# Kernel tuning notes

Hardware: AMD Instinct MI355X
Metric: run time of the kernel (lower is better)

The kernel has to match this reference:

```python
import jax, jax.numpy as jnp
import numpy as np

B, N, H = 512, 128, 256      # graphs, nodes per graph, hidden
NH, HD = 8, 32               # heads, head dim
DEG = 8
E = B * N * DEG              # 524288 edges
BN_EPS = 1e-5


def setup_inputs() -> dict:
    key = jax.random.key(0)
    ks = jax.random.split(key, 16)

    def w(k, shape):
        return jax.random.normal(k, shape, dtype=jnp.float32) * 0.02

    # intra-graph random edges: base offset per graph, local src/dst in [0, N)
    base = jnp.repeat(jnp.arange(B, dtype=jnp.int32) * N, N * DEG)
    edge_src = base + jax.random.randint(ks[1], (E,), 0, N, dtype=jnp.int32)
    edge_dst = base + jax.random.randint(ks[2], (E,), 0, N, dtype=jnp.int32)

    return {
        "h": jax.random.normal(ks[0], (B * N, H), dtype=jnp.float32),
        "edge_src": edge_src,
        "edge_dst": edge_dst,
        "gin_w1": w(ks[3], (H, H)), "gin_b1": jnp.zeros((H,), jnp.float32),
        "gin_w2": w(ks[4], (H, H)), "gin_b2": jnp.zeros((H,), jnp.float32),
        "attn_in_w": w(ks[5], (3 * H, H)), "attn_in_b": jnp.zeros((3 * H,), jnp.float32),
        "attn_out_w": w(ks[6], (H, H)), "attn_out_b": jnp.zeros((H,), jnp.float32),
        "bn_local_g": jnp.ones((H,), jnp.float32), "bn_local_b": jnp.zeros((H,), jnp.float32),
        "bn_attn_g": jnp.ones((H,), jnp.float32), "bn_attn_b": jnp.zeros((H,), jnp.float32),
        "bn_out_g": jnp.ones((H,), jnp.float32), "bn_out_b": jnp.zeros((H,), jnp.float32),
        "ffn1_w": w(ks[7], (2 * H, H)), "ffn1_b": jnp.zeros((2 * H,), jnp.float32),
        "ffn2_w": w(ks[8], (H, 2 * H)), "ffn2_b": jnp.zeros((H,), jnp.float32),
    }


def _bn(x, g, b):
    # nn.BatchNorm1d training-mode forward: batch stats over node dim, biased var
    mean = jnp.mean(x, axis=0)
    var = jnp.mean(jnp.square(x - mean), axis=0)
    return g * (x - mean) * jax.lax.rsqrt(var + BN_EPS) + b


def _mha(x, in_w, in_b, out_w, out_b):
    # x: [B, N, H]; uniform graphs -> key_padding_mask is all-valid
    qkv = x @ in_w.T + in_b                           # [B, N, 3H]
    q, k, v = jnp.split(qkv, 3, axis=-1)
    def heads(t):
        return t.reshape(B, N, NH, HD).transpose(0, 2, 1, 3)  # [B, NH, N, HD]
    q, k, v = heads(q), heads(k), heads(v)
    scores = jnp.einsum('bhqd,bhkd->bhqk', q, k) / jnp.sqrt(jnp.float32(HD))
    att = jax.nn.softmax(scores, axis=-1)
    o = jnp.einsum('bhqk,bhkd->bhqd', att, v).transpose(0, 2, 1, 3).reshape(B, N, H)
    return o @ out_w.T + out_b


def reference(h, edge_src, edge_dst,
              gin_w1, gin_b1, gin_w2, gin_b2,
              attn_in_w, attn_in_b, attn_out_w, attn_out_b,
              bn_local_g, bn_local_b, bn_attn_g, bn_attn_b, bn_out_g, bn_out_b,
              ffn1_w, ffn1_b, ffn2_w, ffn2_b):
    # --- local GIN branch: (1+eps)*h + sum_{j in N(i)} h_j, eps=0, then 2-layer MLP
    agg = jax.ops.segment_sum(h[edge_src], edge_dst, num_segments=B * N)
    z = h + agg
    h_local = jax.nn.relu(z @ gin_w1.T + gin_b1) @ gin_w2.T + gin_b2
    h_local = _bn(h + h_local, bn_local_g, bn_local_b)

    # --- global attention branch (to_dense_batch is an exact reshape here)
    h_dense = h.reshape(B, N, H)
    h_attn = _mha(h_dense, attn_in_w, attn_in_b, attn_out_w, attn_out_b).reshape(B * N, H)
    h_attn = _bn(h + h_attn, bn_attn_g, bn_attn_b)

    # --- combine + FFN + out norm
    x = h_local + h_attn
    x = x + jax.nn.relu(x @ ffn1_w.T + ffn1_b) @ ffn2_w.T + ffn2_b
    return _bn(x, bn_out_g, bn_out_b)
```

## Files before the change

kernel.cpp:

```cpp
#include <hip/hip_runtime.h>
#include <hip/hip_bf16.h>

#define B_   512
#define N_   128
#define H_   256
#define NH_  8
#define HD_  32
#define DEG_ 8
#define R_   (B_ * N_)
#define E_   (B_ * N_ * DEG_)
#define EPG_ (N_ * DEG_)

typedef unsigned short u16;
typedef unsigned int u32;

typedef __attribute__((ext_vector_type(8))) short s16x8;
typedef __attribute__((ext_vector_type(4))) float f32x4;

__device__ __forceinline__ float b2f(u16 u) {
  union { u32 i; float f; } v;
  v.i = ((u32)u) << 16;
  return v.f;
}
__device__ __forceinline__ u16 f2b(float f) {
  union { float f; u32 u; } v;
  v.f = f;
  u32 r = (v.u + 0x7fffu + ((v.u >> 16) & 1u)) >> 16;
  return (u16)r;
}
__device__ __forceinline__ void ld4b(const u16* p, float* o) {
  ushort4 v = *(const ushort4*)p;
  o[0] = b2f(v.x); o[1] = b2f(v.y); o[2] = b2f(v.z); o[3] = b2f(v.w);
}


#define OFF_GW1 0
#define OFF_GB1 65536
#define OFF_GW2 65792
#define OFF_GB2 131328
#define OFF_AIW 131584
#define OFF_AIB 328192
#define OFF_AOW 328960
#define OFF_AOB 394496
#define OFF_F1W 394752
#define OFF_F1B 525824
#define OFF_F2W 526336
#define OFF_F2B 657408
#define W_TOTAL 657664

__global__ void zero_stats(float* __restrict__ st) {
  st[blockIdx.x * 256 + threadIdx.x] = 0.f;
}

__global__ __launch_bounds__(256) void cvt_h(const float* __restrict__ src,
                                             u16* __restrict__ dst) {
  const size_t i = ((size_t)blockIdx.x * 256 + threadIdx.x) * 4;
  const float4 v = *(const float4*)(src + i);
  ushort4 o;
  o.x = f2b(v.x); o.y = f2b(v.y); o.z = f2b(v.z); o.w = f2b(v.w);
  *(ushort4*)(dst + i) = o;
}

__global__ __launch_bounds__(256) void cvt_w(
    const float* s0, const float* s1, const float* s2, const float* s3,
    const float* s4, const float* s5, const float* s6, const float* s7,
    const float* s8, const float* s9, const float* s10, const float* s11,
    u16* __restrict__ dst) {
  const int sizes[12] = {65536, 256, 65536, 256, 196608, 768,
                         65536, 256, 131072, 512, 131072, 256};
  const float* srcs[12] = {s0, s1, s2, s3, s4, s5, s6, s7, s8, s9, s10, s11};
  int gid = (blockIdx.x * 256 + threadIdx.x) * 4;
  if (gid >= W_TOTAL) return;
  int seg = 0, off = gid;
  while (off >= sizes[seg]) { off -= sizes[seg]; seg++; }
  const float4 v = *(const float4*)(srcs[seg] + off);
  ushort4 o;
  o.x = f2b(v.x); o.y = f2b(v.y); o.z = f2b(v.z); o.w = f2b(v.w);
  *(ushort4*)(dst + gid) = o;
}

#define SROWS_ 32

__global__ __launch_bounds__(256) void agg_kernel(
    const u16* __restrict__ h, const int* __restrict__ esrc,
    const int* __restrict__ edst, u16* __restrict__ z) {
  __shared__ int s_src[EPG_];
  __shared__ int s_cnt[SROWS_];
  __shared__ int s_off[SROWS_ + 1];
  __shared__ int s_pos[SROWS_];
  const int g = blockIdx.x;
  const int r0 = blockIdx.y * SROWS_;
  const int t = threadIdx.x;

  if (t < SROWS_) s_cnt[t] = 0;
  __syncthreads();

  const int ebase = g * EPG_;
  int dl[4], sg[4];
#pragma unroll
  for (int i = 0; i < 4; i++) {
    const int e = ebase + t + i * 256;
    sg[i] = esrc[e];
    dl[i] = edst[e] - g * N_ - r0;
    if ((unsigned)dl[i] < SROWS_) atomicAdd(&s_cnt[dl[i]], 1);
  }
  __syncthreads();
  if (t == 0) {
    int acc = 0;
#pragma unroll
    for (int i = 0; i < SROWS_; i++) { s_off[i] = acc; acc += s_cnt[i]; }
    s_off[SROWS_] = acc;
  }
  __syncthreads();
  if (t < SROWS_) s_pos[t] = s_off[t];
  __syncthreads();
#pragma unroll
  for (int i = 0; i < 4; i++) {
    if ((unsigned)dl[i] < SROWS_) {
      const int slot = atomicAdd(&s_pos[dl[i]], 1);
      s_src[slot] = sg[i];
    }
  }
  __syncthreads();

  const int rg = t >> 5;
  const int c0 = (t & 31) * 8;
  for (int ib = 0; ib < SROWS_; ib += 8) {
    const int i = ib + rg;
    const int row = g * N_ + r0 + i;
    float acc[8];
    {
      const s16x8 v = *(const s16x8*)(h + (size_t)row * H_ + c0);
#pragma unroll
      for (int j = 0; j < 8; j++) acc[j] = b2f((u16)v[j]);
    }
    const int e0 = s_off[i], e1 = s_off[i + 1];
    for (int e = e0; e < e1; e++) {
      const int src = s_src[e];
      const s16x8 v = *(const s16x8*)(h + (size_t)src * H_ + c0);
#pragma unroll
      for (int j = 0; j < 8; j++) acc[j] += b2f((u16)v[j]);
    }
    s16x8 o;
#pragma unroll
    for (int j = 0; j < 8; j++) o[j] = (short)f2b(acc[j]);
    *(s16x8*)(z + (size_t)row * H_ + c0) = o;
  }
}

template <int NC, int K, int RELU, int RES, int STATS, int ASPLIT, int CMODE>
__global__ __launch_bounds__(256) void gemm_mfma(
    const u16* A, const u16* A2,
    const u16* __restrict__ W, const u16* __restrict__ bias,
    const u16* res, u16* C0, u16* C1, u16* C2,
    float* __restrict__ gsum, float* __restrict__ gsq) {
  __shared__ u16 As[2][128 * 64] __attribute__((aligned(16)));
  __shared__ u16 Bs[2][128 * 64] __attribute__((aligned(16)));

  const int t = threadIdx.x;
  const int wave = t >> 6, lane = t & 63;
  const int wr = wave >> 1, wc = wave & 1;
  const int quad = lane >> 4, ln15 = lane & 15;
  const int row0 = blockIdx.x * 128, col0 = blockIdx.y * 128;

  f32x4 acc[4][4];
#pragma unroll
  for (int i = 0; i < 4; i++)
#pragma unroll
    for (int j = 0; j < 4; j++) acc[i][j] = (f32x4){0.f, 0.f, 0.f, 0.f};

  auto stage = [&](int b, int kt) {
#pragma unroll
    for (int i = 0; i < 4; i++) {
      const int fid = t + i * 256;
      const int row = fid >> 3;
      const int segp = (fid & 7) ^ (row & 7);
      const u16* Ab;
      int kb;
      if (ASPLIT) {
        if (kt < 256) { Ab = A; kb = kt; } else { Ab = A2; kb = kt - 256; }
      } else {
        Ab = A; kb = kt;
      }
      const int astr = ASPLIT ? 256 : K;
      const u16* ga = Ab + (size_t)(row0 + row) * astr + kb + segp * 8;
      __builtin_amdgcn_global_load_lds(
          (const __attribute__((address_space(1))) void*)ga,
          (__attribute__((address_space(3))) void*)(&As[b][fid * 8]), 16, 0, 0);
      const u16* gw = W + (size_t)(col0 + row) * K + kt + segp * 8;
      __builtin_amdgcn_global_load_lds(
          (const __attribute__((address_space(1))) void*)gw,
          (__attribute__((address_space(3))) void*)(&Bs[b][fid * 8]), 16, 0, 0);
    }
  };

  stage(0, 0);
  for (int kt = 0; kt < K; kt += 64) {
    const int cur = (kt >> 6) & 1;
    if (kt + 64 < K) {
      stage(cur ^ 1, kt + 64);
      asm volatile("s_waitcnt vmcnt(8)" ::: "memory");
    } else {
      asm volatile("s_waitcnt vmcnt(0)" ::: "memory");
    }
    __builtin_amdgcn_s_barrier();
#pragma unroll
    for (int ks = 0; ks < 64; ks += 32) {
      s16x8 af[4], bf[4];
#pragma unroll
      for (int i = 0; i < 4; i++) {
        const int ra = wr * 64 + i * 16 + ln15;
        af[i] = *(const s16x8*)(
            &As[cur][ra * 64 + ((((ks >> 3) + quad) ^ (ra & 7)) * 8)]);
      }
#pragma unroll
      for (int j = 0; j < 4; j++) {
        const int rb = wc * 64 + j * 16 + ln15;
        bf[j] = *(const s16x8*)(
            &Bs[cur][rb * 64 + ((((ks >> 3) + quad) ^ (rb & 7)) * 8)]);
      }
#pragma unroll
      for (int i = 0; i < 4; i++)
#pragma unroll
        for (int j = 0; j < 4; j++)
          acc[i][j] = __builtin_amdgcn_mfma_f32_16x16x32_bf16(af[i], bf[j], acc[i][j], 0, 0, 0);
    }
    __builtin_amdgcn_s_barrier();
  }

  const int cbase = col0 + wc * 64;
  u16* Cb;
  int coff, cstr;
  if (CMODE) {
    const int chunk = col0 >> 8;
    Cb = (chunk == 0) ? C0 : ((chunk == 1) ? C1 : C2);
    coff = (col0 & 255) + wc * 64;
    cstr = 256;
  } else {
    Cb = C0; coff = cbase; cstr = NC;
  }

  float bs[4];
#pragma unroll
  for (int j = 0; j < 4; j++) bs[j] = b2f(bias[cbase + j * 16 + ln15]);

  float ssum[4] = {}, ssq[4] = {};
#pragma unroll
  for (int i = 0; i < 4; i++) {
    const int rbase = row0 + wr * 64 + i * 16 + quad * 4;
#pragma unroll
    for (int reg = 0; reg < 4; reg++) {
      const int row = rbase + reg;
#pragma unroll
      for (int j = 0; j < 4; j++) {
        float val = acc[i][j][reg] + bs[j];
        if (RELU) val = fmaxf(val, 0.f);
        if (RES) val += b2f(res[(size_t)row * 256 + cbase + j * 16 + ln15]);
        Cb[(size_t)row * cstr + coff + j * 16 + ln15] = f2b(val);
        if (STATS) { ssum[j] += val; ssq[j] += val * val; }
      }
    }
  }

  if (STATS) {
#pragma unroll
    for (int j = 0; j < 4; j++) {
      float s = ssum[j];
      s += __shfl_xor(s, 16);
      s += __shfl_xor(s, 32);
      float q = ssq[j];
      q += __shfl_xor(q, 16);
      q += __shfl_xor(q, 32);
      if (lane < 16) {
        atomicAdd(&gsum[cbase + j * 16 + lane], s);
        atomicAdd(&gsq[cbase + j * 16 + lane], q);
      }
    }
  }
}

__global__ __launch_bounds__(256) void attn_mfma(
    const u16* q, const u16* __restrict__ k,
    const u16* __restrict__ v, u16* o) {
  __shared__ u16 lds[21760] __attribute__((aligned(16)));
  u16* Vt = lds;
  u16* Qs = lds + 4352;
  u16* Ks = lds + 4352 + 5120;
  u16* P  = lds + 4352;

  const int g = blockIdx.x >> 3;
  const int hd = blockIdx.x & 7;
  const int t = threadIdx.x;
  const int wave = t >> 6, lane = t & 63;
  const int quad = lane >> 4, ln15 = lane & 15;
  const int strip = wave * 32;
  const float scale = 0.1767766952966369f;

#pragma unroll
  for (int i = 0; i < 4; i++) {
    const int fid = t + i * 256;
    const int row = fid >> 3;
    const int seg = fid & 7;
    const size_t gidx = (size_t)(g * N_ + row) * H_ + hd * HD_ + seg * 4;
    const ushort4 qv = *(const ushort4*)(q + gidx);
    const ushort4 kv = *(const ushort4*)(k + gidx);
    const ushort4 vv = *(const ushort4*)(v + gidx);
    ushort4 qs;
    qs.x = f2b(b2f(qv.x) * scale); qs.y = f2b(b2f(qv.y) * scale);
    qs.z = f2b(b2f(qv.z) * scale); qs.w = f2b(b2f(qv.w) * scale);
    *(ushort4*)(Qs + row * 40 + seg * 4) = qs;
    *(ushort4*)(Ks + row * 40 + seg * 4) = kv;
    Vt[(seg * 4 + 0) * 136 + row] = vv.x;
    Vt[(seg * 4 + 1) * 136 + row] = vv.y;
    Vt[(seg * 4 + 2) * 136 + row] = vv.z;
    Vt[(seg * 4 + 3) * 136 + row] = vv.w;
  }
  __syncthreads();

  s16x8 af[2], bf[8];
#pragma unroll
  for (int mi = 0; mi < 2; mi++)
    af[mi] = *(const s16x8*)(Qs + (strip + mi * 16 + ln15) * 40 + quad * 8);
#pragma unroll
  for (int nj = 0; nj < 8; nj++)
    bf[nj] = *(const s16x8*)(Ks + (nj * 16 + ln15) * 40 + quad * 8);

  f32x4 acc[2][8];
#pragma unroll
  for (int mi = 0; mi < 2; mi++)
#pragma unroll
    for (int nj = 0; nj < 8; nj++)
      acc[mi][nj] = __builtin_amdgcn_mfma_f32_16x16x32_bf16(
          af[mi], bf[nj], (f32x4){0.f, 0.f, 0.f, 0.f}, 0, 0, 0);

  __syncthreads();

#pragma unroll
  for (int mi = 0; mi < 2; mi++) {
#pragma unroll
    for (int reg = 0; reg < 4; reg++) {
      float mx = acc[mi][0][reg];
#pragma unroll
      for (int j = 1; j < 8; j++) mx = fmaxf(mx, acc[mi][j][reg]);
      mx = fmaxf(mx, __shfl_xor(mx, 1));
      mx = fmaxf(mx, __shfl_xor(mx, 2));
      mx = fmaxf(mx, __shfl_xor(mx, 4));
      mx = fmaxf(mx, __shfl_xor(mx, 8));
      float e[8], s = 0.f;
#pragma unroll
      for (int j = 0; j < 8; j++) { e[j] = __expf(acc[mi][j][reg] - mx); s += e[j]; }
      s += __shfl_xor(s, 1);
      s += __shfl_xor(s, 2);
      s += __shfl_xor(s, 4);
      s += __shfl_xor(s, 8);
      const float inv = 1.f / s;
      const int prow = strip + mi * 16 + quad * 4 + reg;
#pragma unroll
      for (int j = 0; j < 8; j++)
        P[prow * 136 + j * 16 + ln15] = f2b(e[j] * inv);
    }
  }
  __syncthreads();

  f32x4 acc2[2][2];
#pragma unroll
  for (int mi = 0; mi < 2; mi++)
#pragma unroll
    for (int nj = 0; nj < 2; nj++) acc2[mi][nj] = (f32x4){0.f, 0.f, 0.f, 0.f};
#pragma unroll
  for (int kt = 0; kt < 4; kt++) {
    s16x8 paf[2], vbf[2];
#pragma unroll
    for (int mi = 0; mi < 2; mi++)
      paf[mi] = *(const s16x8*)(P + (strip + mi * 16 + ln15) * 136 + kt * 32 + quad * 8);
#pragma unroll
    for (int nj = 0; nj < 2; nj++)
      vbf[nj] = *(const s16x8*)(Vt + (nj * 16 + ln15) * 136 + kt * 32 + quad * 8);
#pragma unroll
    for (int mi = 0; mi < 2; mi++)
#pragma unroll
      for (int nj = 0; nj < 2; nj++)
        acc2[mi][nj] = __builtin_amdgcn_mfma_f32_16x16x32_bf16(
            paf[mi], vbf[nj], acc2[mi][nj], 0, 0, 0);
  }

#pragma unroll
  for (int mi = 0; mi < 2; mi++)
#pragma unroll
    for (int nj = 0; nj < 2; nj++)
#pragma unroll
      for (int reg = 0; reg < 4; reg++) {
        const int row = strip + mi * 16 + quad * 4 + reg;
        o[(size_t)(g * N_ + row) * H_ + hd * HD_ + nj * 16 + ln15] =
            f2b(acc2[mi][nj][reg]);
      }
}

__global__ void bn_finalize(const float* __restrict__ sum,
                            const float* __restrict__ sq,
                            const float* __restrict__ g,
                            const float* __restrict__ bb,
                            float* __restrict__ a, float* __restrict__ b) {
  const int c = threadIdx.x;
  const float mean = sum[c] * (1.f / R_);
  const float var = fmaxf(sq[c] * (1.f / R_) - mean * mean, 0.f);
  const float ai = g[c] * rsqrtf(var + 1e-5f);
  a[c] = ai;
  b[c] = bb[c] - mean * ai;
}

__global__ __launch_bounds__(256) void combine_kernel(
    const u16* __restrict__ rl, const u16* __restrict__ ra,
    const float* __restrict__ st, u16* __restrict__ x) {
  const size_t i = (size_t)blockIdx.x * 256 + threadIdx.x;
  const int col = (int)(i & 63) * 4;
  float rl4[4], ra4[4];
  ld4b(rl + i * 4, rl4);
  ld4b(ra + i * 4, ra4);
  const float* al = st + 1536;
  const float* bl = st + 1792;
  const float* aa = st + 2048;
  const float* ba = st + 2304;
  ushort4 o;
  u16* ov = (u16*)&o;
#pragma unroll
  for (int j = 0; j < 4; j++)
    ov[j] = f2b(al[col + j] * rl4[j] + bl[col + j] + aa[col + j] * ra4[j] + ba[col + j]);
  *(ushort4*)(x + i * 4) = o;
}

__global__ __launch_bounds__(256) void final_kernel(
    const u16* __restrict__ y, const float* __restrict__ st,
    float* __restrict__ out) {
  const size_t i = (size_t)blockIdx.x * 256 + threadIdx.x;
  const int col = (int)(i & 63) * 4;
  float y4[4];
  ld4b(y + i * 4, y4);
  const float* ao = st + 2560;
  const float* bo = st + 2816;
  float4 o;
  o.x = ao[col + 0] * y4[0] + bo[col + 0];
  o.y = ao[col + 1] * y4[1] + bo[col + 1];
  o.z = ao[col + 2] * y4[2] + bo[col + 2];
  o.w = ao[col + 3] * y4[3] + bo[col + 3];
  *(float4*)(out + i * 4) = o;
}

extern "C" void kernel_launch(void* const* d_in, const int* in_sizes, int n_in,
                              void* d_out, int out_size, void* d_ws, size_t ws_size,
                              hipStream_t stream) {
  const float* h = (const float*)d_in[0];
  const int* esrc = (const int*)d_in[1];
  const int* edst = (const int*)d_in[2];
  const float* bn_local_g = (const float*)d_in[11];
  const float* bn_local_b = (const float*)d_in[12];
  const float* bn_attn_g = (const float*)d_in[13];
  const float* bn_attn_b = (const float*)d_in[14];
  const float* bn_out_g = (const float*)d_in[15];
  const float* bn_out_b = (const float*)d_in[16];

  const size_t RH = (size_t)R_ * H_;
  float* stats = (float*)d_ws;
  u16* WB = (u16*)((char*)d_ws + 65536);
  u16* Hb = (u16*)((char*)d_ws + 65536 + 2097152);
  u16* S1 = Hb + RH;
  u16* S2 = S1 + RH;
  u16* OD = (u16*)d_out;
  float* outf = (float*)d_out;

  zero_stats<<<12, 256, 0, stream>>>(stats);
  cvt_h<<<(int)(RH / 4 / 256), 256, 0, stream>>>(h, Hb);
  cvt_w<<<(W_TOTAL / 4 + 255) / 256, 256, 0, stream>>>(
      (const float*)d_in[3], (const float*)d_in[4], (const float*)d_in[5],
      (const float*)d_in[6], (const float*)d_in[7], (const float*)d_in[8],
      (const float*)d_in[9], (const float*)d_in[10], (const float*)d_in[17],
      (const float*)d_in[18], (const float*)d_in[19], (const float*)d_in[20], WB);

  gemm_mfma<768, 256, 0, 0, 0, 0, 1><<<dim3(512, 6), 256, 0, stream>>>(
      Hb, nullptr, WB + OFF_AIW, WB + OFF_AIB, nullptr, S1, S2, OD, nullptr, nullptr);
  attn_mfma<<<B_ * NH_, 256, 0, stream>>>(S1, S2, OD, S1);
  gemm_mfma<256, 256, 0, 1, 1, 0, 0><<<dim3(512, 2), 256, 0, stream>>>(
      S1, nullptr, WB + OFF_AOW, WB + OFF_AOB, Hb, S2, nullptr, nullptr,
      stats + 512, stats + 768);
  agg_kernel<<<dim3(B_, 4), 256, 0, stream>>>(Hb, esrc, edst, OD);
  gemm_mfma<256, 256, 1, 0, 0, 0, 0><<<dim3(512, 2), 256, 0, stream>>>(
      OD, nullptr, WB + OFF_GW1, WB + OFF_GB1, nullptr, S1, nullptr, nullptr,
      nullptr, nullptr);
  gemm_mfma<256, 256, 0, 1, 1, 0, 0><<<dim3(512, 2), 256, 0, stream>>>(
      S1, nullptr, WB + OFF_GW2, WB + OFF_GB2, Hb, OD, nullptr, nullptr,
      stats + 0, stats + 256);

  bn_finalize<<<1, 256, 0, stream>>>(stats + 0, stats + 256, bn_local_g,
                                     bn_local_b, stats + 1536, stats + 1792);
  bn_finalize<<<1, 256, 0, stream>>>(stats + 512, stats + 768, bn_attn_g,
                                     bn_attn_b, stats + 2048, stats + 2304);

  combine_kernel<<<(int)(RH / 4 / 256), 256, 0, stream>>>(OD, S2, stats, S1);
  gemm_mfma<512, 256, 1, 0, 0, 0, 1><<<dim3(512, 4), 256, 0, stream>>>(
      S1, nullptr, WB + OFF_F1W, WB + OFF_F1B, nullptr, S2, OD, nullptr,
      nullptr, nullptr);
  gemm_mfma<256, 512, 0, 1, 1, 1, 0><<<dim3(512, 2), 256, 0, stream>>>(
      S2, OD, WB + OFF_F2W, WB + OFF_F2B, S1, S1, nullptr, nullptr,
      stats + 1024, stats + 1280);

  bn_finalize<<<1, 256, 0, stream>>>(stats + 1024, stats + 1280, bn_out_g,
                                     bn_out_b, stats + 2560, stats + 2816);
  final_kernel<<<(int)(RH / 4 / 256), 256, 0, stream>>>(S1, stats, outf);
}
```

Baseline: 608.6 us.

## Store bf16 activations in GEMM-tile swizzled layout for contiguous A staging

Result: no change. 612.9 us (+0.7%).

```diff
diff --git a/kernel.cpp b/kernel.cpp
--- a/kernel.cpp
+++ b/kernel.cpp
@@ -31,6 +31,11 @@
 __device__ __forceinline__ void ld4b(const u16* p, float* o) {
   ushort4 v = *(const ushort4*)p;
   o[0] = b2f(v.x); o[1] = b2f(v.y); o[2] = b2f(v.z); o[3] = b2f(v.w);
+}
+
+__device__ __forceinline__ int tix(int row, int col) {
+  return ((row >> 7) << 15) + (((col >> 6) & 3) << 13) + ((row & 127) << 6) +
+         (((((col >> 3) & 7) ^ (row & 7))) << 3) + (col & 7);
 }
 
 
@@ -54,11 +59,11 @@
 
 __global__ __launch_bounds__(256) void cvt_h(const float* __restrict__ src,
                                              u16* __restrict__ dst) {
-  const size_t i = ((size_t)blockIdx.x * 256 + threadIdx.x) * 4;
-  const float4 v = *(const float4*)(src + i);
+  const int e = (blockIdx.x * 256 + threadIdx.x) * 4;
+  const float4 v = *(const float4*)(src + e);
   ushort4 o;
   o.x = f2b(v.x); o.y = f2b(v.y); o.z = f2b(v.z); o.w = f2b(v.w);
-  *(ushort4*)(dst + i) = o;
+  *(ushort4*)(dst + tix(e >> 8, e & 255)) = o;
 }
 
 __global__ __launch_bounds__(256) void cvt_w(
@@ -130,21 +135,21 @@
     const int row = g * N_ + r0 + i;
     float acc[8];
     {
-      const s16x8 v = *(const s16x8*)(h + (size_t)row * H_ + c0);
+      const s16x8 v = *(const s16x8*)(h + tix(row, c0));
 #pragma unroll
       for (int j = 0; j < 8; j++) acc[j] = b2f((u16)v[j]);
     }
     const int e0 = s_off[i], e1 = s_off[i + 1];
     for (int e = e0; e < e1; e++) {
       const int src = s_src[e];
-      const s16x8 v = *(const s16x8*)(h + (size_t)src * H_ + c0);
+      const s16x8 v = *(const s16x8*)(h + tix(src, c0));
 #pragma unroll
       for (int j = 0; j < 8; j++) acc[j] += b2f((u16)v[j]);
     }
     s16x8 o;
 #pragma unroll
     for (int j = 0; j < 8; j++) o[j] = (short)f2b(acc[j]);
-    *(s16x8*)(z + (size_t)row * H_ + c0) = o;
+    *(s16x8*)(z + tix(row, c0)) = o;
   }
 }
 
@@ -170,23 +175,22 @@
     for (int j = 0; j < 4; j++) acc[i][j] = (f32x4){0.f, 0.f, 0.f, 0.f};
 
   auto stage = [&](int b, int kt) {
+    const u16* Ab;
+    int ksl;
+    if (ASPLIT) {
+      if (kt < 256) { Ab = A; ksl = kt >> 6; } else { Ab = A2; ksl = (kt - 256) >> 6; }
+    } else {
+      Ab = A; ksl = kt >> 6;
+    }
+    const u16* abase = Ab + ((size_t)blockIdx.x << 15) + (ksl << 13);
 #pragma unroll
     for (int i = 0; i < 4; i++) {
       const int fid = t + i * 256;
+      __builtin_amdgcn_global_load_lds(
+          (const __attribute__((address_space(1))) void*)(abase + fid * 8),
+          (__attribute__((address_space(3))) void*)(&As[b][fid * 8]), 16, 0, 0);
       const int row = fid >> 3;
       const int segp = (fid & 7) ^ (row & 7);
-      const u16* Ab;
-      int kb;
-      if (ASPLIT) {
-        if (kt < 256) { Ab = A; kb = kt; } else { Ab = A2; kb = kt - 256; }
-      } else {
-        Ab = A; kb = kt;
-      }
-      const int astr = ASPLIT ? 256 : K;
-      const u16* ga = Ab + (size_t)(row0 + row) * astr + kb + segp * 8;
-      __builtin_amdgcn_global_load_lds(
-          (const __attribute__((address_space(1))) void*)ga,
-          (__attribute__((address_space(3))) void*)(&As[b][fid * 8]), 16, 0, 0);
       const u16* gw = W + (size_t)(col0 + row) * K + kt + segp * 8;
       __builtin_amdgcn_global_load_lds(
           (const __attribute__((address_space(1))) void*)gw,
@@ -230,14 +234,13 @@
 
   const int cbase = col0 + wc * 64;
   u16* Cb;
-  int coff, cstr;
+  int coff;
   if (CMODE) {
     const int chunk = col0 >> 8;
     Cb = (chunk == 0) ? C0 : ((chunk == 1) ? C1 : C2);
     coff = (col0 & 255) + wc * 64;
-    cstr = 256;
   } else {
-    Cb = C0; coff = cbase; cstr = NC;
+    Cb = C0; coff = cbase;
   }
 
   float bs[4];
@@ -255,8 +258,8 @@
       for (int j = 0; j < 4; j++) {
         float val = acc[i][j][reg] + bs[j];
         if (RELU) val = fmaxf(val, 0.f);
-        if (RES) val += b2f(res[(size_t)row * 256 + cbase + j * 16 + ln15]);
-        Cb[(size_t)row * cstr + coff + j * 16 + ln15] = f2b(val);
+        if (RES) val += b2f(res[tix(row, cbase + j * 16 + ln15)]);
+        Cb[tix(row, coff + j * 16 + ln15)] = f2b(val);
         if (STATS) { ssum[j] += val; ssq[j] += val * val; }
       }
     }
@@ -301,7 +304,7 @@
     const int fid = t + i * 256;
     const int row = fid >> 3;
     const int seg = fid & 7;
-    const size_t gidx = (size_t)(g * N_ + row) * H_ + hd * HD_ + seg * 4;
+    const int gidx = tix(g * N_ + row, hd * HD_ + seg * 4);
     const ushort4 qv = *(const ushort4*)(q + gidx);
     const ushort4 kv = *(const ushort4*)(k + gidx);
     const ushort4 vv = *(const ushort4*)(v + gidx);
@@ -391,7 +394,7 @@
 #pragma unroll
       for (int reg = 0; reg < 4; reg++) {
         const int row = strip + mi * 16 + quad * 4 + reg;
-        o[(size_t)(g * N_ + row) * H_ + hd * HD_ + nj * 16 + ln15] =
+        o[tix(g * N_ + row, hd * HD_ + nj * 16 + ln15)] =
             f2b(acc2[mi][nj][reg]);
       }
 }
@@ -412,11 +415,12 @@
 __global__ __launch_bounds__(256) void combine_kernel(
     const u16* __restrict__ rl, const u16* __restrict__ ra,
     const float* __restrict__ st, u16* __restrict__ x) {
-  const size_t i = (size_t)blockIdx.x * 256 + threadIdx.x;
-  const int col = (int)(i & 63) * 4;
+  const int e = (blockIdx.x * 256 + threadIdx.x) * 4;
+  const int col = e & 255;
+  const int idx = tix(e >> 8, col);
   float rl4[4], ra4[4];
-  ld4b(rl + i * 4, rl4);
-  ld4b(ra + i * 4, ra4);
+  ld4b(rl + idx, rl4);
+  ld4b(ra + idx, ra4);
   const float* al = st + 1536;
   const float* bl = st + 1792;
   const float* aa = st + 2048;
@@ -426,16 +430,16 @@
 #pragma unroll
   for (int j = 0; j < 4; j++)
     ov[j] = f2b(al[col + j] * rl4[j] + bl[col + j] + aa[col + j] * ra4[j] + ba[col + j]);
-  *(ushort4*)(x + i * 4) = o;
+  *(ushort4*)(x + idx) = o;
 }
 
 __global__ __launch_bounds__(256) void final_kernel(
     const u16* __restrict__ y, const float* __restrict__ st,
     float* __restrict__ out) {
-  const size_t i = (size_t)blockIdx.x * 256 + threadIdx.x;
-  const int col = (int)(i & 63) * 4;
+  const int e = (blockIdx.x * 256 + threadIdx.x) * 4;
+  const int col = e & 255;
   float y4[4];
-  ld4b(y + i * 4, y4);
+  ld4b(y + tix(e >> 8, col), y4);
   const float* ao = st + 2560;
   const float* bo = st + 2816;
   float4 o;
@@ -443,7 +447,7 @@
   o.y = ao[col + 1] * y4[1] + bo[col + 1];
   o.z = ao[col + 2] * y4[2] + bo[col + 2];
   o.w = ao[col + 3] * y4[3] + bo[col + 3];
-  *(float4*)(out + i * 4) = o;
+  *(float4*)(out + e) = o;
 }
 
 extern "C" void kernel_launch(void* const* d_in, const int* in_sizes, int n_in,
```
